# Kernel optimization log

Hardware: AMD Instinct MI355X
Metric: run time of the kernel (lower is better)

The kernel has to match this reference:

```python
import jax, jax.numpy as jnp
import numpy as np

EPS_LN = 1e-5
EPS_SUM = 1e-5


def setup_inputs() -> dict:
    key = jax.random.key(0)
    ks = jax.random.split(key, 6)
    B, T, F, D = 8, 1024, 512, 64
    x = jax.random.normal(ks[0], (B, T, F), dtype=jnp.float32)
    state = jnp.zeros((B, 1, D * D), dtype=jnp.float32)
    s = 1.0 / np.sqrt(F)
    Wk = jax.random.uniform(ks[1], (F, D), jnp.float32, -s, s)
    Wq = jax.random.uniform(ks[2], (F, D), jnp.float32, -s, s)
    Wv = jax.random.uniform(ks[3], (F, D), jnp.float32, -s, s)
    gamma = jnp.ones((F,), jnp.float32)
    beta = jnp.zeros((F,), jnp.float32)
    return {"x": x, "state": state, "Wk": Wk, "Wq": Wq, "Wv": Wv,
            "gamma": gamma, "beta": beta}


def _layernorm(x, gamma, beta):
    mu = jnp.mean(x, axis=-1, keepdims=True)
    var = jnp.mean(jnp.square(x - mu), axis=-1, keepdims=True)
    return (x - mu) * jax.lax.rsqrt(var + EPS_LN) * gamma + beta


def reference(x, state, Wk, Wq, Wv, gamma, beta):
    B, T, F = x.shape
    D = Wk.shape[1]
    xn = _layernorm(x, gamma, beta)
    K = jax.nn.relu(xn @ Wk)            # [B,T,D]
    Q = jax.nn.relu(xn @ Wq)
    V = xn @ Wv
    # sum normalization (paper)
    K = K / (EPS_SUM + jnp.sum(K, axis=-1, keepdims=True))
    Q = Q / (EPS_SUM + jnp.sum(Q, axis=-1, keepdims=True))
    # outer-product fast weights per step: kv[b,t,i,j] = V[b,t,i] * K[b,t,j]
    kv = jnp.einsum('bti,btj->btij', V, K)        # [B,T,D,D]
    # 'sum' aggregator: running (cumulative) sum seeded by the initial state
    state_seq = state.reshape(B, 1, D, D) + jnp.cumsum(kv, axis=1)  # [B,T,D,D]
    y = jnp.einsum('btij,bti->btj', state_seq, Q)  # [B,T,D]
    return (y, state_seq)
```

## Files before the change

kernel.cpp:

```cpp
#include <hip/hip_runtime.h>

#define BB 8
#define TT 1024
#define FF 512
#define DD 64
#define LCH 16
#define CCH (TT / LCH)
#define SEG 8
#define NSEG (CCH / SEG)
#define EE (DD * DD)

__device__ __forceinline__ float wave_sum64(float v) {
  #pragma unroll
  for (int m = 32; m >= 1; m >>= 1) v += __shfl_xor(v, m, 64);
  return v;
}

__global__ __launch_bounds__(256) void lnprojcs_k(
    const float* __restrict__ x,
    const float* __restrict__ gamma, const float* __restrict__ beta,
    const float* __restrict__ Wk, const float* __restrict__ Wq,
    const float* __restrict__ Wv,
    float* __restrict__ Ko, float* __restrict__ Qo, float* __restrict__ Vo,
    float* __restrict__ S) {
  __shared__ float lx[LCH * FF];
  __shared__ float part[4 * LCH * 3 * DD];
  const int tid = threadIdx.x;
  const int wv = tid >> 6, lane = tid & 63;
  const int bc = blockIdx.x;
  const size_t row0 = (size_t)bc * LCH;

  {
    const float4* xg = (const float4*)(x + row0 * FF);
    float4* lx4 = (float4*)lx;
    #pragma unroll
    for (int i = 0; i < (LCH * FF / 4) / 256; ++i)
      lx4[tid + 256 * i] = xg[tid + 256 * i];
  }
  __syncthreads();

  {
    float g[FF / 64], bt[FF / 64];
    #pragma unroll
    for (int k = 0; k < FF / 64; ++k) {
      g[k]  = gamma[lane + 64 * k];
      bt[k] = beta[lane + 64 * k];
    }
    #pragma unroll
    for (int rr = 0; rr < LCH / 4; ++rr) {
      int r = wv * (LCH / 4) + rr;
      float v[FF / 64];
      float s = 0.f, ss = 0.f;
      #pragma unroll
      for (int k = 0; k < FF / 64; ++k) {
        v[k] = lx[r * FF + lane + 64 * k];
        s += v[k]; ss += v[k] * v[k];
      }
      s = wave_sum64(s); ss = wave_sum64(ss);
      float m = s * (1.f / FF);
      float var = ss * (1.f / FF) - m * m;
      float rs = rsqrtf(var + 1e-5f);
      #pragma unroll
      for (int k = 0; k < FF / 64; ++k)
        lx[r * FF + lane + 64 * k] = (v[k] - m) * rs * g[k] + bt[k];
    }
  }
  __syncthreads();

  float acc[LCH][3];
  #pragma unroll
  for (int r = 0; r < LCH; ++r)
    #pragma unroll
    for (int p = 0; p < 3; ++p) acc[r][p] = 0.f;

  const int fbase = wv * (FF / 4);
  #pragma unroll 2
  for (int f0 = fbase; f0 < fbase + FF / 4; f0 += 4) {
    float wk0 = Wk[(f0 + 0) * DD + lane], wk1 = Wk[(f0 + 1) * DD + lane];
    float wk2 = Wk[(f0 + 2) * DD + lane], wk3 = Wk[(f0 + 3) * DD + lane];
    float wq0 = Wq[(f0 + 0) * DD + lane], wq1 = Wq[(f0 + 1) * DD + lane];
    float wq2 = Wq[(f0 + 2) * DD + lane], wq3 = Wq[(f0 + 3) * DD + lane];
    float wv0 = Wv[(f0 + 0) * DD + lane], wv1 = Wv[(f0 + 1) * DD + lane];
    float wv2 = Wv[(f0 + 2) * DD + lane], wv3 = Wv[(f0 + 3) * DD + lane];
    #pragma unroll
    for (int r = 0; r < LCH; ++r) {
      float4 xv = *(const float4*)&lx[r * FF + f0];
      acc[r][0] += (xv.x * wk0 + xv.y * wk1) + (xv.z * wk2 + xv.w * wk3);
      acc[r][1] += (xv.x * wq0 + xv.y * wq1) + (xv.z * wq2 + xv.w * wq3);
      acc[r][2] += (xv.x * wv0 + xv.y * wv1) + (xv.z * wv2 + xv.w * wv3);
    }
  }

  #pragma unroll
  for (int r = 0; r < LCH; ++r)
    #pragma unroll
    for (int p = 0; p < 3; ++p)
      part[((wv * LCH + r) * 3 + p) * DD + lane] = acc[r][p];
  __syncthreads();

  float* lk = lx;
  float* lv = lx + LCH * DD;
  #pragma unroll
  for (int i = 0; i < 12; ++i) {
    int pid = wv * 12 + i;
    int r = pid / 3, p = pid - r * 3;
    float val = part[((0 * LCH + r) * 3 + p) * DD + lane]
              + part[((1 * LCH + r) * 3 + p) * DD + lane]
              + part[((2 * LCH + r) * 3 + p) * DD + lane]
              + part[((3 * LCH + r) * 3 + p) * DD + lane];
    if (p < 2) {
      val = fmaxf(val, 0.f);
      float sm = wave_sum64(val);
      val = val / (1e-5f + sm);
    }
    float* outp = (p == 0) ? Ko : (p == 1) ? Qo : Vo;
    outp[(row0 + r) * DD + lane] = val;
    if (p == 0) lk[r * DD + lane] = val;
    else if (p == 2) lv[r * DD + lane] = val;
  }
  __syncthreads();

  {
    int j = lane, i0 = wv << 4;
    float a2[16];
    #pragma unroll
    for (int ii = 0; ii < 16; ++ii) a2[ii] = 0.f;
    for (int t = 0; t < LCH; ++t) {
      float kj = lk[t * DD + j];
      #pragma unroll
      for (int ii = 0; ii < 16; ++ii) a2[ii] += lv[t * DD + i0 + ii] * kj;
    }
    float* Sp = S + (size_t)bc * EE;
    #pragma unroll
    for (int ii = 0; ii < 16; ++ii) Sp[(i0 + ii) * DD + j] = a2[ii];
  }
}

__global__ __launch_bounds__(256) void allprefix_k(const float* __restrict__ S,
                                                   const float* __restrict__ st0,
                                                   float* __restrict__ P) {
  int blk = blockIdx.x;
  int b = blk >> 7;
  int seg = (blk >> 4) & 7;
  int e = ((blk & 15) << 8) + threadIdx.x;
  const float* Sb = S + (size_t)b * CCH * EE + e;
  float run = st0[(size_t)b * EE + e];
  const int nprev = seg * SEG;
  float r0 = 0.f, r1 = 0.f, r2 = 0.f, r3 = 0.f;
  for (int c = 0; c < nprev; c += 4) {
    r0 += Sb[(size_t)(c + 0) * EE];
    r1 += Sb[(size_t)(c + 1) * EE];
    r2 += Sb[(size_t)(c + 2) * EE];
    r3 += Sb[(size_t)(c + 3) * EE];
  }
  run += (r0 + r1) + (r2 + r3);
  const float* Ss = Sb + (size_t)nprev * EE;
  float sv[SEG];
  #pragma unroll
  for (int c = 0; c < SEG; ++c) sv[c] = Ss[(size_t)c * EE];
  float* Pb = P + ((size_t)b * CCH + nprev) * EE + e;
  #pragma unroll
  for (int c = 0; c < SEG; ++c) {
    Pb[(size_t)c * EE] = run;
    run += sv[c];
  }
}

__global__ __launch_bounds__(256) void scan_k(const float* __restrict__ Kx,
                     const float* __restrict__ Qx, const float* __restrict__ Vx,
                     const float* __restrict__ P,
                     float* __restrict__ y, float* __restrict__ sout) {
  int bc = blockIdx.x, tid = threadIdx.x;
  int wv = tid >> 6, j = tid & 63;
  int i0 = wv * 16;
  __shared__ float yp[4][LCH][DD];
  float S[16];
  const float* Pp = P + (size_t)bc * EE;
  #pragma unroll
  for (int ii = 0; ii < 16; ++ii) S[ii] = Pp[(i0 + ii) * DD + j];
  const float* Kb = Kx + (size_t)bc * LCH * DD;
  const float* Vb = Vx + (size_t)bc * LCH * DD;
  const float* Qb = Qx + (size_t)bc * LCH * DD;
  float kreg[LCH];
  #pragma unroll
  for (int t = 0; t < LCH; ++t) kreg[t] = Kb[t * DD + j];
  float* so = sout + (size_t)bc * LCH * EE + (size_t)i0 * DD + j;
  for (int t = 0; t < LCH; ++t) {
    const float* Vt = Vb + t * DD + i0;
    const float* Qt = Qb + t * DD + i0;
    float kj = kreg[t];
    float y0 = 0.f, y1 = 0.f, y2 = 0.f, y3 = 0.f;
    float* sot = so + (size_t)t * EE;
    #pragma unroll
    for (int ii = 0; ii < 16; ii += 4) {
      S[ii]     += Vt[ii]     * kj; sot[(ii)     * DD] = S[ii];     y0 += S[ii]     * Qt[ii];
      S[ii + 1] += Vt[ii + 1] * kj; sot[(ii + 1) * DD] = S[ii + 1]; y1 += S[ii + 1] * Qt[ii + 1];
      S[ii + 2] += Vt[ii + 2] * kj; sot[(ii + 2) * DD] = S[ii + 2]; y2 += S[ii + 2] * Qt[ii + 2];
      S[ii + 3] += Vt[ii + 3] * kj; sot[(ii + 3) * DD] = S[ii + 3]; y3 += S[ii + 3] * Qt[ii + 3];
    }
    yp[wv][t][j] = (y0 + y1) + (y2 + y3);
  }
  __syncthreads();
  float* yo = y + (size_t)bc * LCH * DD;
  #pragma unroll
  for (int tt = 0; tt < LCH / 4; ++tt) {
    int t = wv * (LCH / 4) + tt;
    yo[t * DD + j] = (yp[0][t][j] + yp[1][t][j]) + (yp[2][t][j] + yp[3][t][j]);
  }
}

extern "C" void kernel_launch(void* const* d_in, const int* in_sizes, int n_in,
                              void* d_out, int out_size, void* d_ws, size_t ws_size,
                              hipStream_t stream) {
  const float* x     = (const float*)d_in[0];
  const float* st0   = (const float*)d_in[1];
  const float* Wk    = (const float*)d_in[2];
  const float* Wq    = (const float*)d_in[3];
  const float* Wv    = (const float*)d_in[4];
  const float* gamma = (const float*)d_in[5];
  const float* beta  = (const float*)d_in[6];

  float* out  = (float*)d_out;
  float* yout = out;
  float* sseq = out + (size_t)BB * TT * DD;

  float* ws = (float*)d_ws;
  float* Ko = ws;
  float* Qo = Ko + (size_t)BB * TT * DD;
  float* Vo = Qo + (size_t)BB * TT * DD;
  float* S  = Vo + (size_t)BB * TT * DD;
  float* P  = S  + (size_t)BB * CCH * EE;

  lnprojcs_k<<<BB * CCH, 256, 0, stream>>>(x, gamma, beta, Wk, Wq, Wv, Ko, Qo, Vo, S);
  allprefix_k<<<BB * NSEG * 16, 256, 0, stream>>>(S, st0, P);
  scan_k    <<<BB * CCH, 256, 0, stream>>>(Ko, Qo, Vo, P, yout, sseq);
}
```

Baseline: 212.3 us.

## Fuse three kernels into one cooperative kernel with grid sync

Merges the LN/projection, chunk-prefix and scan kernels into a single cooperative kernel that keeps K, Q and V in shared memory and syncs the grid after writing per-chunk state sums. Each block then sums all preceding chunk states itself, which removes the P buffer and the K/Q/V round trips through global memory. It also uses nontemporal stores for the large state_seq output and reuses one shared buffer to cut LDS use. The cost is a linear prefix whose length grows with chunk index (up to 63 reads of 16 KB per block), a grid-wide barrier, and a launch that needs all 512 blocks to be resident at once.

```diff
diff --git a/kernel.cpp b/kernel.cpp
--- a/kernel.cpp
+++ b/kernel.cpp
@@ -1,4 +1,7 @@
 #include <hip/hip_runtime.h>
+#include <hip/hip_cooperative_groups.h>
+
+namespace cg = cooperative_groups;
 
 #define BB 8
 #define TT 1024
@@ -6,8 +9,6 @@
 #define DD 64
 #define LCH 16
 #define CCH (TT / LCH)
-#define SEG 8
-#define NSEG (CCH / SEG)
 #define EE (DD * DD)
 
 __device__ __forceinline__ float wave_sum64(float v) {
@@ -16,43 +17,48 @@
   return v;
 }
 
-__global__ __launch_bounds__(256) void lnprojcs_k(
-    const float* __restrict__ x,
-    const float* __restrict__ gamma, const float* __restrict__ beta,
+__global__ __launch_bounds__(256) void fused_k(
+    const float* __restrict__ x, const float* __restrict__ st0,
     const float* __restrict__ Wk, const float* __restrict__ Wq,
     const float* __restrict__ Wv,
-    float* __restrict__ Ko, float* __restrict__ Qo, float* __restrict__ Vo,
-    float* __restrict__ S) {
-  __shared__ float lx[LCH * FF];
-  __shared__ float part[4 * LCH * 3 * DD];
+    const float* __restrict__ gamma, const float* __restrict__ beta,
+    float* __restrict__ S, float* __restrict__ y, float* __restrict__ sseq) {
+  __shared__ float smem[9216];
+  float* lx   = smem;
+  float* part = smem;
+  float* lk   = smem + 6144;
+  float* lq   = smem + 7168;
+  float* lv   = smem + 8192;
+
   const int tid = threadIdx.x;
   const int wv = tid >> 6, lane = tid & 63;
   const int bc = blockIdx.x;
+  const int b = bc >> 6, c = bc & (CCH - 1);
   const size_t row0 = (size_t)bc * LCH;
 
   {
     const float4* xg = (const float4*)(x + row0 * FF);
     float4* lx4 = (float4*)lx;
     #pragma unroll
-    for (int i = 0; i < (LCH * FF / 4) / 256; ++i)
+    for (int i = 0; i < 8; ++i)
       lx4[tid + 256 * i] = xg[tid + 256 * i];
   }
   __syncthreads();
 
   {
-    float g[FF / 64], bt[FF / 64];
-    #pragma unroll
-    for (int k = 0; k < FF / 64; ++k) {
+    float g[8], bt[8];
+    #pragma unroll
+    for (int k = 0; k < 8; ++k) {
       g[k]  = gamma[lane + 64 * k];
       bt[k] = beta[lane + 64 * k];
     }
     #pragma unroll
-    for (int rr = 0; rr < LCH / 4; ++rr) {
-      int r = wv * (LCH / 4) + rr;
-      float v[FF / 64];
+    for (int rr = 0; rr < 4; ++rr) {
+      int r = wv * 4 + rr;
+      float v[8];
       float s = 0.f, ss = 0.f;
       #pragma unroll
-      for (int k = 0; k < FF / 64; ++k) {
+      for (int k = 0; k < 8; ++k) {
         v[k] = lx[r * FF + lane + 64 * k];
         s += v[k]; ss += v[k] * v[k];
       }
@@ -61,7 +67,7 @@
       float var = ss * (1.f / FF) - m * m;
       float rs = rsqrtf(var + 1e-5f);
       #pragma unroll
-      for (int k = 0; k < FF / 64; ++k)
+      for (int k = 0; k < 8; ++k)
         lx[r * FF + lane + 64 * k] = (v[k] - m) * rs * g[k] + bt[k];
     }
   }
@@ -90,122 +96,99 @@
       acc[r][2] += (xv.x * wv0 + xv.y * wv1) + (xv.z * wv2 + xv.w * wv3);
     }
   }
+  __syncthreads();
 
   #pragma unroll
-  for (int r = 0; r < LCH; ++r)
-    #pragma unroll
-    for (int p = 0; p < 3; ++p)
-      part[((wv * LCH + r) * 3 + p) * DD + lane] = acc[r][p];
-  __syncthreads();
-
-  float* lk = lx;
-  float* lv = lx + LCH * DD;
-  #pragma unroll
-  for (int i = 0; i < 12; ++i) {
-    int pid = wv * 12 + i;
-    int r = pid / 3, p = pid - r * 3;
-    float val = part[((0 * LCH + r) * 3 + p) * DD + lane]
-              + part[((1 * LCH + r) * 3 + p) * DD + lane]
-              + part[((2 * LCH + r) * 3 + p) * DD + lane]
-              + part[((3 * LCH + r) * 3 + p) * DD + lane];
-    if (p < 2) {
-      val = fmaxf(val, 0.f);
-      float sm = wave_sum64(val);
-      val = val / (1e-5f + sm);
-    }
-    float* outp = (p == 0) ? Ko : (p == 1) ? Qo : Vo;
-    outp[(row0 + r) * DD + lane] = val;
-    if (p == 0) lk[r * DD + lane] = val;
-    else if (p == 2) lv[r * DD + lane] = val;
-  }
-  __syncthreads();
-
-  {
-    int j = lane, i0 = wv << 4;
+  for (int h = 0; h < 2; ++h) {
+    #pragma unroll
+    for (int r = 0; r < 8; ++r)
+      #pragma unroll
+      for (int p = 0; p < 3; ++p)
+        part[((wv * 8 + r) * 3 + p) * DD + lane] = acc[h * 8 + r][p];
+    __syncthreads();
+    #pragma unroll
+    for (int i = 0; i < 6; ++i) {
+      int pid = wv * 6 + i;
+      int r = pid / 3, p = pid - r * 3;
+      float val = part[((0 * 8 + r) * 3 + p) * DD + lane]
+                + part[((1 * 8 + r) * 3 + p) * DD + lane]
+                + part[((2 * 8 + r) * 3 + p) * DD + lane]
+                + part[((3 * 8 + r) * 3 + p) * DD + lane];
+      if (p < 2) {
+        val = fmaxf(val, 0.f);
+        float sm = wave_sum64(val);
+        val = val / (1e-5f + sm);
+      }
+      int rg = h * 8 + r;
+      if (p == 0)      lk[rg * DD + lane] = val;
+      else if (p == 1) lq[rg * DD + lane] = val;
+      else             lv[rg * DD + lane] = val;
+    }
+    __syncthreads();
+  }
+
+  {
+    const int j = lane, s0 = wv << 4;
     float a2[16];
     #pragma unroll
     for (int ii = 0; ii < 16; ++ii) a2[ii] = 0.f;
+    #pragma unroll
     for (int t = 0; t < LCH; ++t) {
       float kj = lk[t * DD + j];
       #pragma unroll
-      for (int ii = 0; ii < 16; ++ii) a2[ii] += lv[t * DD + i0 + ii] * kj;
+      for (int ii = 0; ii < 16; ++ii) a2[ii] += lv[t * DD + s0 + ii] * kj;
     }
     float* Sp = S + (size_t)bc * EE;
     #pragma unroll
-    for (int ii = 0; ii < 16; ++ii) Sp[(i0 + ii) * DD + j] = a2[ii];
-  }
-}
-
-__global__ __launch_bounds__(256) void allprefix_k(const float* __restrict__ S,
-                                                   const float* __restrict__ st0,
-                                                   float* __restrict__ P) {
-  int blk = blockIdx.x;
-  int b = blk >> 7;
-  int seg = (blk >> 4) & 7;
-  int e = ((blk & 15) << 8) + threadIdx.x;
-  const float* Sb = S + (size_t)b * CCH * EE + e;
-  float run = st0[(size_t)b * EE + e];
-  const int nprev = seg * SEG;
-  float r0 = 0.f, r1 = 0.f, r2 = 0.f, r3 = 0.f;
-  for (int c = 0; c < nprev; c += 4) {
-    r0 += Sb[(size_t)(c + 0) * EE];
-    r1 += Sb[(size_t)(c + 1) * EE];
-    r2 += Sb[(size_t)(c + 2) * EE];
-    r3 += Sb[(size_t)(c + 3) * EE];
-  }
-  run += (r0 + r1) + (r2 + r3);
-  const float* Ss = Sb + (size_t)nprev * EE;
-  float sv[SEG];
-  #pragma unroll
-  for (int c = 0; c < SEG; ++c) sv[c] = Ss[(size_t)c * EE];
-  float* Pb = P + ((size_t)b * CCH + nprev) * EE + e;
-  #pragma unroll
-  for (int c = 0; c < SEG; ++c) {
-    Pb[(size_t)c * EE] = run;
-    run += sv[c];
-  }
-}
-
-__global__ __launch_bounds__(256) void scan_k(const float* __restrict__ Kx,
-                     const float* __restrict__ Qx, const float* __restrict__ Vx,
-                     const float* __restrict__ P,
-                     float* __restrict__ y, float* __restrict__ sout) {
-  int bc = blockIdx.x, tid = threadIdx.x;
-  int wv = tid >> 6, j = tid & 63;
-  int i0 = wv * 16;
-  __shared__ float yp[4][LCH][DD];
-  float S[16];
-  const float* Pp = P + (size_t)bc * EE;
-  #pragma unroll
-  for (int ii = 0; ii < 16; ++ii) S[ii] = Pp[(i0 + ii) * DD + j];
-  const float* Kb = Kx + (size_t)bc * LCH * DD;
-  const float* Vb = Vx + (size_t)bc * LCH * DD;
-  const float* Qb = Qx + (size_t)bc * LCH * DD;
-  float kreg[LCH];
-  #pragma unroll
-  for (int t = 0; t < LCH; ++t) kreg[t] = Kb[t * DD + j];
-  float* so = sout + (size_t)bc * LCH * EE + (size_t)i0 * DD + j;
-  for (int t = 0; t < LCH; ++t) {
-    const float* Vt = Vb + t * DD + i0;
-    const float* Qt = Qb + t * DD + i0;
-    float kj = kreg[t];
-    float y0 = 0.f, y1 = 0.f, y2 = 0.f, y3 = 0.f;
-    float* sot = so + (size_t)t * EE;
-    #pragma unroll
-    for (int ii = 0; ii < 16; ii += 4) {
-      S[ii]     += Vt[ii]     * kj; sot[(ii)     * DD] = S[ii];     y0 += S[ii]     * Qt[ii];
-      S[ii + 1] += Vt[ii + 1] * kj; sot[(ii + 1) * DD] = S[ii + 1]; y1 += S[ii + 1] * Qt[ii + 1];
-      S[ii + 2] += Vt[ii + 2] * kj; sot[(ii + 2) * DD] = S[ii + 2]; y2 += S[ii + 2] * Qt[ii + 2];
-      S[ii + 3] += Vt[ii + 3] * kj; sot[(ii + 3) * DD] = S[ii + 3]; y3 += S[ii + 3] * Qt[ii + 3];
-    }
-    yp[wv][t][j] = (y0 + y1) + (y2 + y3);
-  }
-  __syncthreads();
-  float* yo = y + (size_t)bc * LCH * DD;
-  #pragma unroll
-  for (int tt = 0; tt < LCH / 4; ++tt) {
-    int t = wv * (LCH / 4) + tt;
-    yo[t * DD + j] = (yp[0][t][j] + yp[1][t][j]) + (yp[2][t][j] + yp[3][t][j]);
+    for (int ii = 0; ii < 16; ++ii) Sp[(s0 + ii) * DD + j] = a2[ii];
+  }
+
+  __threadfence();
+  cg::this_grid().sync();
+
+  const int i0 = wv << 4;
+  float run[16];
+  {
+    const float* s0p = st0 + (size_t)b * EE;
+    #pragma unroll
+    for (int ii = 0; ii < 16; ++ii) run[ii] = s0p[(i0 + ii) * DD + lane];
+    const float* Sb = S + (size_t)b * CCH * EE;
+    for (int cc = 0; cc < c; ++cc) {
+      const float* Sc = Sb + (size_t)cc * EE;
+      #pragma unroll
+      for (int ii = 0; ii < 16; ++ii) run[ii] += Sc[(i0 + ii) * DD + lane];
+    }
+  }
+
+  float* yp = smem;
+  {
+    const int j = lane;
+    float* so = sseq + (size_t)bc * LCH * EE + (size_t)i0 * DD + j;
+    for (int t = 0; t < LCH; ++t) {
+      float kj = lk[t * DD + j];
+      float* sot = so + (size_t)t * EE;
+      float y0 = 0.f, y1 = 0.f, y2 = 0.f, y3 = 0.f;
+      #pragma unroll
+      for (int q4 = 0; q4 < 4; ++q4) {
+        float4 vt = *(const float4*)&lv[t * DD + i0 + q4 * 4];
+        float4 qt = *(const float4*)&lq[t * DD + i0 + q4 * 4];
+        run[q4*4+0] += vt.x * kj; __builtin_nontemporal_store(run[q4*4+0], &sot[(q4*4+0) * DD]); y0 += run[q4*4+0] * qt.x;
+        run[q4*4+1] += vt.y * kj; __builtin_nontemporal_store(run[q4*4+1], &sot[(q4*4+1) * DD]); y1 += run[q4*4+1] * qt.y;
+        run[q4*4+2] += vt.z * kj; __builtin_nontemporal_store(run[q4*4+2], &sot[(q4*4+2) * DD]); y2 += run[q4*4+2] * qt.z;
+        run[q4*4+3] += vt.w * kj; __builtin_nontemporal_store(run[q4*4+3], &sot[(q4*4+3) * DD]); y3 += run[q4*4+3] * qt.w;
+      }
+      yp[(wv * LCH + t) * DD + j] = (y0 + y1) + (y2 + y3);
+    }
+  }
+  __syncthreads();
+  {
+    float* yo = y + (size_t)bc * LCH * DD;
+    #pragma unroll
+    for (int tt = 0; tt < 4; ++tt) {
+      int t = wv * 4 + tt;
+      yo[t * DD + lane] = (yp[(0 * LCH + t) * DD + lane] + yp[(1 * LCH + t) * DD + lane])
+                        + (yp[(2 * LCH + t) * DD + lane] + yp[(3 * LCH + t) * DD + lane]);
+    }
   }
 }
 
@@ -224,14 +207,11 @@
   float* yout = out;
   float* sseq = out + (size_t)BB * TT * DD;
 
-  float* ws = (float*)d_ws;
-  float* Ko = ws;
-  float* Qo = Ko + (size_t)BB * TT * DD;
-  float* Vo = Qo + (size_t)BB * TT * DD;
-  float* S  = Vo + (size_t)BB * TT * DD;
-  float* P  = S  + (size_t)BB * CCH * EE;
-
-  lnprojcs_k<<<BB * CCH, 256, 0, stream>>>(x, gamma, beta, Wk, Wq, Wv, Ko, Qo, Vo, S);
-  allprefix_k<<<BB * NSEG * 16, 256, 0, stream>>>(S, st0, P);
-  scan_k    <<<BB * CCH, 256, 0, stream>>>(Ko, Qo, Vo, P, yout, sseq);
+  float* Sbuf = (float*)d_ws;
+
+  void* args[] = {(void*)&x, (void*)&st0, (void*)&Wk, (void*)&Wq, (void*)&Wv,
+                  (void*)&gamma, (void*)&beta, (void*)&Sbuf, (void*)&yout,
+                  (void*)&sseq};
+  hipLaunchCooperativeKernel((void*)fused_k, dim3(BB * CCH), dim3(256),
+                             args, 0, stream);
 }
```

Measured after the change: 313.2 us. 1.48x slower.
